# Performance work log

Hardware: AMD Instinct MI355X
Metric: run time of the kernel (lower is better)

Reference implementation:

```python
import jax, jax.numpy as jnp
import numpy as np

H = 16  # num_heads

def setup_inputs() -> dict:
    key = jax.random.key(0)
    k1, k2, k3 = jax.random.split(key, 3)
    D = 1024
    x = jax.random.normal(k1, (4, 2048, D), dtype=jnp.float32)
    W_qkv = jax.random.normal(k2, (D, 3 * D), dtype=jnp.float32) * (1.0 / np.sqrt(D))
    b_qkv = jnp.zeros((3 * D,), dtype=jnp.float32)
    W_out = jax.random.normal(k3, (D, D), dtype=jnp.float32) * (1.0 / np.sqrt(D))
    b_out = jnp.zeros((D,), dtype=jnp.float32)
    return {"x": x, "W_qkv": W_qkv, "b_qkv": b_qkv, "W_out": W_out, "b_out": b_out}

def reference(x, W_qkv, b_qkv, W_out, b_out):
    B, S, D = x.shape
    hd = D // H  # head_dim
    qkv = x @ W_qkv + b_qkv  # [B,S,3D]
    q, k, v = jnp.split(qkv, 3, axis=-1)
    # [B,S,D] -> [B,H,S,hd]
    q = q.reshape(B, S, H, hd).transpose(0, 2, 1, 3)
    k = k.reshape(B, S, H, hd).transpose(0, 2, 1, 3)
    v = v.reshape(B, S, H, hd).transpose(0, 2, 1, 3)
    scores = jnp.einsum('bhqd,bhkd->bhqk', q, k) / jnp.sqrt(jnp.float32(hd))
    weights = jax.nn.softmax(scores, axis=-1)  # dropout p=0.0 (eval)
    out = jnp.einsum('bhqk,bhkd->bhqd', weights, v)
    out = out.transpose(0, 2, 1, 3).reshape(B, S, D)
    return out @ W_out + b_out
```

## Files before the change

kernel.cpp:

```cpp
#include <hip/hip_runtime.h>

typedef __bf16 bf16;
typedef __bf16 bf16x4 __attribute__((ext_vector_type(4)));
typedef __bf16 bf16x8 __attribute__((ext_vector_type(8)));
typedef float f32x4 __attribute__((ext_vector_type(4)));
typedef unsigned u32x2 __attribute__((ext_vector_type(2)));

static constexpr int NB = 4;
static constexpr int NS = 2048;
static constexpr int ND = 1024;
static constexpr int NH = 16;
static constexpr int HD = 64;
static constexpr float QSCALE = 0.18033688011112042f;

#define GL16(g, l)                                                             \
    __builtin_amdgcn_global_load_lds(                                          \
        (const __attribute__((address_space(1))) void*)(g),                    \
        (__attribute__((address_space(3))) void*)(l), 16, 0, 0)

static __device__ __forceinline__ unsigned pk2(float a, float b) {
    union { __bf16 h[2]; unsigned u; } t;
    t.h[0] = (__bf16)a; t.h[1] = (__bf16)b;
    return t.u;
}

__global__ void k_conv(const float* __restrict__ in, bf16* __restrict__ out, int n) {
    int i = (blockIdx.x * blockDim.x + threadIdx.x) * 4;
    if (i < n) {
        float4 v = *reinterpret_cast<const float4*>(in + i);
        bf16* o = out + i;
        o[0] = (bf16)v.x; o[1] = (bf16)v.y; o[2] = (bf16)v.z; o[3] = (bf16)v.w;
    }
}

__global__ void k_transconv(const float* __restrict__ in, bf16* __restrict__ out,
                            int K, int N) {
    __shared__ float tile[64][33];
    int k0 = blockIdx.y * 64, n0 = blockIdx.x * 32;
    int tx = threadIdx.x, ty = threadIdx.y;
#pragma unroll
    for (int i = 0; i < 8; ++i)
        tile[ty + 8 * i][tx] = in[(long)(k0 + ty + 8 * i) * N + n0 + tx];
    __syncthreads();
    int t = ty * 32 + tx;
    int row = t >> 3;
    int col8 = (t & 7) * 8;
    bf16x8 v;
#pragma unroll
    for (int c = 0; c < 8; ++c) v[c] = (bf16)tile[col8 + c][row];
    *reinterpret_cast<bf16x8*>(&out[(long)(n0 + row) * K + k0 + col8]) = v;
}

template <int MODE>
__global__ __launch_bounds__(256, 2) void k_gemm(
    const bf16* __restrict__ A, const bf16* __restrict__ Bt,
    const float* __restrict__ bias,
    void* __restrict__ out0, void* __restrict__ out1,
    int M, int Kd)
{
    constexpr int BM = 128, BN = 128, BK = 64;
    __shared__ __align__(16) bf16 As[2][BM * BK];
    __shared__ __align__(16) bf16 Bs[2][BN * BK];

    const int t = threadIdx.x;
    const int wid = t >> 6, lane = t & 63;
    const int wm = wid >> 1, wn = wid & 1;
    const int m0 = blockIdx.y * BM, n0 = blockIdx.x * BN;
    const int lrow = lane & 15, lhi = lane >> 4;

    const int srow0 = wid * 32 + (lane >> 3);
    const int scol = ((lane & 7) ^ (lane >> 3)) * 8;
    const bf16* ag = A + (long)(m0 + srow0) * Kd + scol;
    const bf16* bg = Bt + (long)(n0 + srow0) * Kd + scol;

    auto STAGE = [&](int buf_, int k0_) {
#pragma unroll
        for (int c = 0; c < 4; ++c) {
            GL16(ag + (long)(c * 8) * Kd + k0_, &As[buf_][(wid * 32 + c * 8) * BK]);
            GL16(bg + (long)(c * 8) * Kd + k0_, &Bs[buf_][(wid * 32 + c * 8) * BK]);
        }
    };

    f32x4 acc[4][4] = {};
    const int nt = Kd >> 6;
    const int swzr = (lrow & 7) << 4;
    int co[2];
#pragma unroll
    for (int kk = 0; kk < 2; ++kk)
        co[kk] = ((kk * 64 + lhi * 16) ^ swzr) >> 1;

    STAGE(0, 0);
    int cur = 0;
    for (int tix = 0; tix < nt; ++tix) {
        if (tix + 1 < nt) {
            STAGE(cur ^ 1, (tix + 1) * BK);
            asm volatile("s_waitcnt vmcnt(8)" ::: "memory");
        } else {
            asm volatile("s_waitcnt vmcnt(0)" ::: "memory");
        }
        __builtin_amdgcn_s_barrier();
        __builtin_amdgcn_sched_barrier(0);

        bf16x8 af[2][4], bfr[2][4];
#pragma unroll
        for (int kk = 0; kk < 2; ++kk)
#pragma unroll
            for (int i = 0; i < 4; ++i) {
                af[kk][i]  = *reinterpret_cast<const bf16x8*>(
                    &As[cur][(wm * 64 + i * 16 + lrow) * BK + co[kk]]);
                bfr[kk][i] = *reinterpret_cast<const bf16x8*>(
                    &Bs[cur][(wn * 64 + i * 16 + lrow) * BK + co[kk]]);
            }
        __builtin_amdgcn_s_setprio(1);
#pragma unroll
        for (int kk = 0; kk < 2; ++kk)
#pragma unroll
            for (int i = 0; i < 4; ++i)
#pragma unroll
                for (int j = 0; j < 4; ++j) {
                    if (MODE == 1)
                        acc[i][j] = __builtin_amdgcn_mfma_f32_16x16x32_bf16(
                            af[kk][i], bfr[kk][j], acc[i][j], 0, 0, 0);
                    else
                        acc[i][j] = __builtin_amdgcn_mfma_f32_16x16x32_bf16(
                            bfr[kk][j], af[kk][i], acc[i][j], 0, 0, 0);
                }
        __builtin_amdgcn_s_setprio(0);
        __builtin_amdgcn_s_barrier();
        cur ^= 1;
    }

    const int colbase = n0 + wn * 64;

    if (MODE == 0) {
        bf16* eb = (bf16*)As + wid * 4096;
        const bool isQ = (colbase >> 10) == 0;
#pragma unroll
        for (int j = 0; j < 4; ++j) {
            f32x4 bv = *reinterpret_cast<const f32x4*>(&bias[colbase + j * 16 + 4 * lhi]);
#pragma unroll
            for (int i = 0; i < 4; ++i) {
                int srt = i * 16 + lrow;
                bf16x4 pk;
#pragma unroll
                for (int r = 0; r < 4; ++r) {
                    float v = acc[i][j][r] + bv[r];
                    pk[r] = (bf16)(isQ ? v * QSCALE : v);
                }
                *reinterpret_cast<bf16x4*>(
                    reinterpret_cast<char*>(eb) + srt * 128 +
                    (((j * 16 + 4 * lhi) * 2) ^ ((srt & 7) << 4))) = pk;
            }
        }
        const int h = (colbase & 1023) >> 6;
        bf16* Ob = isQ ? (bf16*)out0 : (bf16*)out1;
#pragma unroll
        for (int it = 0; it < 8; ++it) {
            int rt = it * 8 + (lane >> 3);
            bf16x8 v = *reinterpret_cast<const bf16x8*>(
                reinterpret_cast<char*>(eb) + rt * 128 +
                (((lane & 7) * 16) ^ ((rt & 7) << 4)));
            int row = m0 + wm * 64 + rt;
            int bb = row >> 11, s = row & 2047;
            long bh = (long)bb * NH + h;
            *reinterpret_cast<bf16x8*>(&Ob[(bh * NS + s) * HD + (lane & 7) * 8]) = v;
        }
    } else if (MODE == 1) {
        bf16* eb = (bf16*)As + wid * 4096;
#pragma unroll
        for (int j = 0; j < 4; ++j) {
            float bv = bias[colbase + j * 16 + lrow];
            int drt = j * 16 + lrow;
#pragma unroll
            for (int i = 0; i < 4; ++i) {
                bf16x4 pk;
#pragma unroll
                for (int r = 0; r < 4; ++r) pk[r] = (bf16)(acc[i][j][r] + bv);
                *reinterpret_cast<bf16x4*>(
                    reinterpret_cast<char*>(eb) + drt * 128 +
                    (((i * 16 + 4 * lhi) * 2) ^ ((drt & 7) << 4))) = pk;
            }
        }
        const int h = (colbase & 1023) >> 6;
        const int mrow = m0 + wm * 64;
        const int bb = mrow >> 11, s0 = mrow & 2047;
        bf16* Vt = (bf16*)out0;
#pragma unroll
        for (int it = 0; it < 8; ++it) {
            int dt = it * 8 + (lane >> 3);
            bf16x8 v = *reinterpret_cast<const bf16x8*>(
                reinterpret_cast<char*>(eb) + dt * 128 +
                (((lane & 7) * 16) ^ ((dt & 7) << 4)));
            long bh = (long)bb * NH + h;
            *reinterpret_cast<bf16x8*>(&Vt[(bh * HD + dt) * NS + s0 + (lane & 7) * 8]) = v;
        }
    } else {
        float* ef = (float*)As + wid * 2048;
        float* O = (float*)out0;
#pragma unroll
        for (int half = 0; half < 2; ++half) {
#pragma unroll
            for (int i2 = 0; i2 < 2; ++i2) {
                int i = half * 2 + i2;
                int srt = i2 * 16 + lrow;
#pragma unroll
                for (int j = 0; j < 4; ++j) {
                    f32x4 bv = *reinterpret_cast<const f32x4*>(
                        &bias[colbase + j * 16 + 4 * lhi]);
                    f32x4 v = acc[i][j] + bv;
                    *reinterpret_cast<f32x4*>(
                        reinterpret_cast<char*>(ef) + srt * 256 +
                        (((j * 16 + 4 * lhi) * 4) ^ ((srt & 7) << 4))) = v;
                }
            }
#pragma unroll
            for (int it = 0; it < 8; ++it) {
                int rt = it * 4 + (lane >> 4);
                f32x4 v = *reinterpret_cast<const f32x4*>(
                    reinterpret_cast<char*>(ef) + rt * 256 +
                    (((lane & 15) * 16) ^ ((rt & 7) << 4)));
                int row = m0 + wm * 64 + half * 32 + rt;
                *reinterpret_cast<f32x4*>(
                    &O[(long)row * 1024 + colbase + (lane & 15) * 4]) = v;
            }
            asm volatile("" ::: "memory");
        }
    }
}

__global__ __launch_bounds__(512, 4) void k_attn(
    const bf16* __restrict__ Qb, const bf16* __restrict__ Kb,
    const bf16* __restrict__ Vt, bf16* __restrict__ Ao)
{
    constexpr int KB = 64;
    constexpr int NT = NS / KB;
    __shared__ __align__(16) bf16 Ks[2][KB * HD];
    __shared__ __align__(16) bf16 Vs[2][HD * KB];
    __shared__ __align__(16) bf16 Ps[8 * 16 * 64];

    const int t = threadIdx.x;
    const int wid = t >> 6, lane = t & 63;
    const int lrow = lane & 15, lhi = lane >> 4;

    const int flat = blockIdx.y * gridDim.x + blockIdx.x;
    const int n = (flat & 7) * 64 + (flat >> 3);
    const int bh = n >> 3;
    const int qw = (n & 7) * 256 + wid * 32;

    const bf16* Qg = Qb + ((long)bh * NS + qw) * HD;
    const bf16* Kg = Kb + (long)bh * NS * HD;
    const bf16* Vg = Vt + (long)bh * HD * NS;

    bf16x8 qf[2][2];
#pragma unroll
    for (int qfr = 0; qfr < 2; ++qfr)
#pragma unroll
        for (int c = 0; c < 2; ++c)
            qf[qfr][c] = *reinterpret_cast<const bf16x8*>(
                Qg + (long)(qfr * 16 + lrow) * HD + c * 32 + lhi * 8);

    f32x4 of[2][4] = {};
    float lsum[2] = {0.f, 0.f};

    const int gsr = lane >> 3;
    const int gsc = ((lane & 7) ^ gsr) * 8;
    const int rb = wid * 8;
    auto STAGE = [&](int buf, int kb) {
        GL16(Kg + (long)(kb + rb + gsr) * HD + gsc, &Ks[buf][rb * 64]);
        GL16(Vg + (long)(rb + gsr) * NS + kb + gsc, &Vs[buf][rb * 64]);
    };

    const int rsw = (lrow & 7) << 4;
    bf16* psw = &Ps[wid * 1024 + lrow * 64];

    auto COMPUTE = [&](int b_) {
        f32x4 st[2][4] = {};
        __builtin_amdgcn_s_setprio(1);
#pragma unroll
        for (int j = 0; j < 4; ++j)
#pragma unroll
            for (int c = 0; c < 2; ++c) {
                bf16x8 kf = *reinterpret_cast<const bf16x8*>(
                    &Ks[b_][(j * 16 + lrow) * 64 + (((c * 64 + lhi * 16) ^ rsw) >> 1)]);
#pragma unroll
                for (int qfr = 0; qfr < 2; ++qfr)
                    st[qfr][j] = __builtin_amdgcn_mfma_f32_16x16x32_bf16(
                        kf, qf[qfr][c], st[qfr][j], 0, 0, 0);
            }
        __builtin_amdgcn_s_setprio(0);

        bf16x8 pfr[2][2];
#pragma unroll
        for (int qfr = 0; qfr < 2; ++qfr) {
#pragma unroll
            for (int j = 0; j < 4; ++j) {
                float e0 = __builtin_amdgcn_exp2f(st[qfr][j][0]);
                float e1 = __builtin_amdgcn_exp2f(st[qfr][j][1]);
                float e2 = __builtin_amdgcn_exp2f(st[qfr][j][2]);
                float e3 = __builtin_amdgcn_exp2f(st[qfr][j][3]);
                lsum[qfr] += (e0 + e1) + (e2 + e3);
                u32x2 w; w[0] = pk2(e0, e1); w[1] = pk2(e2, e3);
                *reinterpret_cast<u32x2*>(
                    reinterpret_cast<char*>(psw) + (((j * 32 + lhi * 8) ^ rsw))) = w;
            }
            asm volatile("" ::: "memory");
#pragma unroll
            for (int chunk = 0; chunk < 2; ++chunk)
                pfr[qfr][chunk] = *reinterpret_cast<const bf16x8*>(
                    reinterpret_cast<char*>(psw) + ((chunk * 64 + lhi * 16) ^ rsw));
            asm volatile("" ::: "memory");
        }

        __builtin_amdgcn_s_setprio(1);
#pragma unroll
        for (int chunk = 0; chunk < 2; ++chunk)
#pragma unroll
            for (int f = 0; f < 4; ++f) {
                bf16x8 vf = *reinterpret_cast<const bf16x8*>(
                    &Vs[b_][(f * 16 + lrow) * 64 +
                            (((chunk * 64 + lhi * 16) ^ rsw) >> 1)]);
#pragma unroll
                for (int qfr = 0; qfr < 2; ++qfr)
                    of[qfr][f] = __builtin_amdgcn_mfma_f32_16x16x32_bf16(
                        vf, pfr[qfr][chunk], of[qfr][f], 0, 0, 0);
            }
        __builtin_amdgcn_s_setprio(0);
    };

    STAGE(0, 0);
    int cur = 0;
    for (int it = 0; it < NT; ++it) {
        if (it + 1 < NT) {
            STAGE(cur ^ 1, (it + 1) * KB);
            asm volatile("s_waitcnt vmcnt(2)" ::: "memory");
        } else {
            asm volatile("s_waitcnt vmcnt(0)" ::: "memory");
        }
        __builtin_amdgcn_s_barrier();
        __builtin_amdgcn_sched_barrier(0);
        COMPUTE(cur);
        __builtin_amdgcn_s_barrier();
        cur ^= 1;
    }

#pragma unroll
    for (int qfr = 0; qfr < 2; ++qfr) {
        lsum[qfr] += __shfl_xor(lsum[qfr], 16);
        lsum[qfr] += __shfl_xor(lsum[qfr], 32);
    }

    bf16* eb = (wid < 4) ? ((bf16*)Ks + wid * 2048) : ((bf16*)Vs + (wid - 4) * 2048);
#pragma unroll
    for (int qfr = 0; qfr < 2; ++qfr) {
        float inv = 1.0f / lsum[qfr];
        int srt = qfr * 16 + lrow;
#pragma unroll
        for (int f = 0; f < 4; ++f) {
            bf16x4 pk;
#pragma unroll
            for (int r = 0; r < 4; ++r) pk[r] = (bf16)(of[qfr][f][r] * inv);
            *reinterpret_cast<bf16x4*>(
                reinterpret_cast<char*>(eb) + srt * 128 +
                (((f * 16 + 4 * lhi) * 2) ^ ((srt & 7) << 4))) = pk;
        }
    }
    const int bb = bh >> 4, h = bh & 15;
#pragma unroll
    for (int it = 0; it < 4; ++it) {
        int rt = it * 8 + (lane >> 3);
        bf16x8 v = *reinterpret_cast<const bf16x8*>(
            reinterpret_cast<char*>(eb) + rt * 128 +
            (((lane & 7) * 16) ^ ((rt & 7) << 4)));
        int s = qw + rt;
        *reinterpret_cast<bf16x8*>(
            &Ao[((long)bb * NS + s) * ND + h * HD + (lane & 7) * 8]) = v;
    }
}

extern "C" void kernel_launch(void* const* d_in, const int* in_sizes, int n_in,
                              void* d_out, int out_size, void* d_ws, size_t ws_size,
                              hipStream_t stream) {
    const float* x    = (const float*)d_in[0];
    const float* Wqkv = (const float*)d_in[1];
    const float* bqkv = (const float*)d_in[2];
    const float* Wout = (const float*)d_in[3];
    const float* bout = (const float*)d_in[4];
    float* out = (float*)d_out;

    char* ws = (char*)d_ws;
    bf16* Xb  = (bf16*)(ws);
    bf16* Wqt = (bf16*)(ws + 16777216);
    bf16* Wot = (bf16*)(ws + 23068672);
    bf16* Qb  = (bf16*)(ws + 25165824);
    bf16* Kb  = (bf16*)(ws + 41943040);
    bf16* Vt  = (bf16*)(ws + 58720256);
    bf16* Ab  = (bf16*)(ws + 75497472);

    k_conv<<<dim3(8192), dim3(256), 0, stream>>>(x, Xb, NB * NS * ND);
    k_transconv<<<dim3(96, 16), dim3(32, 8), 0, stream>>>(Wqkv, Wqt, ND, 3 * ND);
    k_transconv<<<dim3(32, 16), dim3(32, 8), 0, stream>>>(Wout, Wot, ND, ND);

    k_gemm<0><<<dim3(16, 64), dim3(256), 0, stream>>>(
        Xb, Wqt, bqkv, Qb, Kb, NB * NS, ND);
    k_gemm<1><<<dim3(8, 64), dim3(256), 0, stream>>>(
        Xb, Wqt + (long)2048 * ND, bqkv + 2048, Vt, nullptr, NB * NS, ND);

    k_attn<<<dim3(8, 64), dim3(512), 0, stream>>>(Qb, Kb, Vt, Ab);

    k_gemm<2><<<dim3(8, 64), dim3(256), 0, stream>>>(
        Ab, Wot, bout, out, nullptr, NB * NS, ND);
}
```

Before: 195.3 us.

## Keep softmax P in registers via 16x16x16 MFMA, permute V^T layout to match

```diff
diff --git a/kernel.cpp b/kernel.cpp
--- a/kernel.cpp
+++ b/kernel.cpp
@@ -3,8 +3,8 @@
 typedef __bf16 bf16;
 typedef __bf16 bf16x4 __attribute__((ext_vector_type(4)));
 typedef __bf16 bf16x8 __attribute__((ext_vector_type(8)));
+typedef short s16x4 __attribute__((ext_vector_type(4)));
 typedef float f32x4 __attribute__((ext_vector_type(4)));
-typedef unsigned u32x2 __attribute__((ext_vector_type(2)));
 
 static constexpr int NB = 4;
 static constexpr int NS = 2048;
@@ -185,14 +185,21 @@
         const int mrow = m0 + wm * 64;
         const int bb = mrow >> 11, s0 = mrow & 2047;
         bf16* Vt = (bf16*)out0;
+        const int pos0 = (lane & 7) * 8;
+        const int k0p = (pos0 >> 5) * 32 + ((pos0 >> 3) & 3) * 4;
 #pragma unroll
         for (int it = 0; it < 8; ++it) {
             int dt = it * 8 + (lane >> 3);
-            bf16x8 v = *reinterpret_cast<const bf16x8*>(
-                reinterpret_cast<char*>(eb) + dt * 128 +
-                (((lane & 7) * 16) ^ ((dt & 7) << 4)));
+            int swz = (dt & 7) << 4;
+            bf16x4 a = *reinterpret_cast<const bf16x4*>(
+                reinterpret_cast<char*>(eb) + dt * 128 + ((2 * k0p) ^ swz));
+            bf16x4 b = *reinterpret_cast<const bf16x4*>(
+                reinterpret_cast<char*>(eb) + dt * 128 + ((2 * (k0p + 16)) ^ swz));
+            bf16x8 v;
+#pragma unroll
+            for (int r = 0; r < 4; ++r) { v[r] = a[r]; v[4 + r] = b[r]; }
             long bh = (long)bb * NH + h;
-            *reinterpret_cast<bf16x8*>(&Vt[(bh * HD + dt) * NS + s0 + (lane & 7) * 8]) = v;
+            *reinterpret_cast<bf16x8*>(&Vt[(bh * HD + dt) * NS + s0 + pos0]) = v;
         }
     } else {
         float* ef = (float*)As + wid * 2048;
@@ -236,7 +243,6 @@
     constexpr int NT = NS / KB;
     __shared__ __align__(16) bf16 Ks[2][KB * HD];
     __shared__ __align__(16) bf16 Vs[2][HD * KB];
-    __shared__ __align__(16) bf16 Ps[8 * 16 * 64];
 
     const int t = threadIdx.x;
     const int wid = t >> 6, lane = t & 63;
@@ -271,7 +277,6 @@
     };
 
     const int rsw = (lrow & 7) << 4;
-    bf16* psw = &Ps[wid * 1024 + lrow * 64];
 
     auto COMPUTE = [&](int b_) {
         f32x4 st[2][4] = {};
@@ -289,9 +294,9 @@
             }
         __builtin_amdgcn_s_setprio(0);
 
-        bf16x8 pfr[2][2];
-#pragma unroll
-        for (int qfr = 0; qfr < 2; ++qfr) {
+        union { unsigned u[2]; s16x4 s; } pj[2][4];
+#pragma unroll
+        for (int qfr = 0; qfr < 2; ++qfr)
 #pragma unroll
             for (int j = 0; j < 4; ++j) {
                 float e0 = __builtin_amdgcn_exp2f(st[qfr][j][0]);
@@ -299,30 +304,26 @@
                 float e2 = __builtin_amdgcn_exp2f(st[qfr][j][2]);
                 float e3 = __builtin_amdgcn_exp2f(st[qfr][j][3]);
                 lsum[qfr] += (e0 + e1) + (e2 + e3);
-                u32x2 w; w[0] = pk2(e0, e1); w[1] = pk2(e2, e3);
-                *reinterpret_cast<u32x2*>(
-                    reinterpret_cast<char*>(psw) + (((j * 32 + lhi * 8) ^ rsw))) = w;
-            }
-            asm volatile("" ::: "memory");
-#pragma unroll
-            for (int chunk = 0; chunk < 2; ++chunk)
-                pfr[qfr][chunk] = *reinterpret_cast<const bf16x8*>(
-                    reinterpret_cast<char*>(psw) + ((chunk * 64 + lhi * 16) ^ rsw));
-            asm volatile("" ::: "memory");
-        }
+                pj[qfr][j].u[0] = pk2(e0, e1);
+                pj[qfr][j].u[1] = pk2(e2, e3);
+            }
 
         __builtin_amdgcn_s_setprio(1);
 #pragma unroll
-        for (int chunk = 0; chunk < 2; ++chunk)
+        for (int p = 0; p < 2; ++p)
 #pragma unroll
             for (int f = 0; f < 4; ++f) {
-                bf16x8 vf = *reinterpret_cast<const bf16x8*>(
+                union { bf16x8 v; s16x4 h[2]; } vf;
+                vf.v = *reinterpret_cast<const bf16x8*>(
                     &Vs[b_][(f * 16 + lrow) * 64 +
-                            (((chunk * 64 + lhi * 16) ^ rsw) >> 1)]);
-#pragma unroll
-                for (int qfr = 0; qfr < 2; ++qfr)
-                    of[qfr][f] = __builtin_amdgcn_mfma_f32_16x16x32_bf16(
-                        vf, pfr[qfr][chunk], of[qfr][f], 0, 0, 0);
+                            (((p * 64 + lhi * 16) ^ rsw) >> 1)]);
+#pragma unroll
+                for (int qfr = 0; qfr < 2; ++qfr) {
+                    of[qfr][f] = __builtin_amdgcn_mfma_f32_16x16x16bf16_1k(
+                        vf.h[0], pj[qfr][2 * p].s, of[qfr][f], 0, 0, 0);
+                    of[qfr][f] = __builtin_amdgcn_mfma_f32_16x16x16bf16_1k(
+                        vf.h[1], pj[qfr][2 * p + 1].s, of[qfr][f], 0, 0, 0);
+                }
             }
         __builtin_amdgcn_s_setprio(0);
     };
```

New measurement: 196.7 us. Within noise of the previous version (+0.7%).
